# Kernel tuning notes

Measured on AMD Instinct MI355X. Metric: run time of the kernel, lower is better.

The kernel has to match this reference:

```python
import jax, jax.numpy as jnp
import numpy as np

N = 6144
M_VID = 1024
M_AUD = 128
APPERTURE = 20
EPS = 1e-6


def setup_inputs() -> dict:
    key = jax.random.key(0)
    ks = jax.random.split(key, 16)
    s = 0.02
    inp = {
        "x": jax.random.normal(ks[0], (1, N, M_VID), dtype=jnp.float32),
        "x_audio": jax.random.normal(ks[1], (1, N, M_AUD), dtype=jnp.float32),
        "seq_len": N,
        "audio_len": N,
        # video self-attention (torch Linear convention: W is [out, in])
        "Wk_v": jax.random.normal(ks[2], (M_VID, M_VID), dtype=jnp.float32) * s,
        "Wq_v": jax.random.normal(ks[3], (M_VID, M_VID), dtype=jnp.float32) * s,
        "Wv_v": jax.random.normal(ks[4], (M_VID, M_VID), dtype=jnp.float32) * s,
        "Wo_v": jax.random.normal(ks[5], (M_VID, M_VID), dtype=jnp.float32) * s,
        # audio self-attention
        "Wk_a": jax.random.normal(ks[6], (M_AUD, M_AUD), dtype=jnp.float32) * s,
        "Wq_a": jax.random.normal(ks[7], (M_AUD, M_AUD), dtype=jnp.float32) * s,
        "Wv_a": jax.random.normal(ks[8], (M_AUD, M_AUD), dtype=jnp.float32) * s,
        "Wo_a": jax.random.normal(ks[9], (M_AUD, M_AUD), dtype=jnp.float32) * s,
        # MLP head
        "ka_w": jax.random.normal(ks[10], (1024, M_VID + M_AUD), dtype=jnp.float32) * s,
        "ka_b": jnp.zeros((1024,), dtype=jnp.float32),
        "kd_w": jax.random.normal(ks[11], (1, 1024), dtype=jnp.float32) * s,
        "kd_b": jnp.zeros((1,), dtype=jnp.float32),
        # layer norms
        "ln_y_g": jnp.ones((M_VID,), dtype=jnp.float32),
        "ln_y_b": jnp.zeros((M_VID,), dtype=jnp.float32),
        "ln_ya_g": jnp.ones((M_AUD,), dtype=jnp.float32),
        "ln_ya_b": jnp.zeros((M_AUD,), dtype=jnp.float32),
        "ln_ka_g": jnp.ones((1024,), dtype=jnp.float32),
        "ln_ka_b": jnp.zeros((1024,), dtype=jnp.float32),
    }
    return inp


def _layer_norm(x, g, b):
    mu = jnp.mean(x, axis=-1, keepdims=True)
    var = jnp.mean((x - mu) ** 2, axis=-1, keepdims=True)
    return (x - mu) / jnp.sqrt(var + EPS) * g + b


def _self_attention(x, Wk, Wq, Wv, Wo):
    # x: [N, d]
    n = x.shape[0]
    K = x @ Wk.T
    Q = (x @ Wq.T) * 0.06
    V = x @ Wv.T
    logits = Q @ K.T  # [N, N]
    # keep only |i-j| < apperture (trimask masks |i-j| >= apperture)
    idx = jnp.arange(n)
    band = jnp.abs(idx[:, None] - idx[None, :]) < APPERTURE
    logits = jnp.where(band, logits, -jnp.inf)
    att = jax.nn.softmax(logits, axis=-1)  # [N, N]
    # torch: y = (V^T @ att)^T == att^T @ V  (note the transpose on att!)
    y = att.T @ V
    return y @ Wo.T, att


def reference(x, x_audio, seq_len, audio_len,
              Wk_v, Wq_v, Wv_v, Wo_v,
              Wk_a, Wq_a, Wv_a, Wo_a,
              ka_w, ka_b, kd_w, kd_b,
              ln_y_g, ln_y_b, ln_ya_g, ln_ya_b, ln_ka_g, ln_ka_b):
    m = x.shape[2]
    m_audio = x_audio.shape[2]
    xf = x.reshape(-1, m)            # [N, 1024]
    xa = x_audio.reshape(-1, m_audio)  # [N, 128]

    y, att_w = _self_attention(xf, Wk_v, Wq_v, Wv_v, Wo_v)
    y = _layer_norm(y + xf, ln_y_g, ln_y_b)

    ya, att_wa = _self_attention(xa, Wk_a, Wq_a, Wv_a, Wo_a)
    ya = _layer_norm(ya + xa, ln_ya_g, ln_ya_b)

    y_comb = jnp.concatenate((y, ya), axis=1)        # [N, 1152]
    att_comb = jnp.concatenate((att_w, att_wa), axis=1)  # [N, 2N]

    h = jax.nn.relu(y_comb @ ka_w.T + ka_b)
    h = _layer_norm(h, ln_ka_g, ln_ka_b)
    score = jax.nn.sigmoid(h @ kd_w.T + kd_b)  # [N, 1]
    score = score.reshape(1, -1)               # [1, N]
    return score, att_comb
```

## Files before the change

kernel.cpp:

```cpp
#include <hip/hip_runtime.h>
#include <stdint.h>

typedef unsigned short u16;
typedef unsigned int u32;
typedef __attribute__((ext_vector_type(8))) short bf16x8;
typedef __attribute__((ext_vector_type(4))) short s16x4;
typedef __attribute__((ext_vector_type(4))) float f32x4;
typedef __attribute__((ext_vector_type(2))) float f32x2;

#define DEV __device__ __forceinline__

DEV u16 f2bf(float f) {
  union { float f; unsigned u; } v; v.f = f;
  unsigned r = v.u + 0x7fffu + ((v.u >> 16) & 1u);
  return (u16)(r >> 16);
}
DEV float bf2f(u16 h) {
  union { u32 u; float f; } v; v.u = ((u32)h) << 16; return v.f;
}
DEV float lo16(u32 w) { union { u32 u; float f; } v; v.u = w << 16; return v.f; }
DEV float hi16(u32 w) { union { u32 u; float f; } v; v.u = w & 0xFFFF0000u; return v.f; }
DEV int imax(int a, int b) { return a > b ? a : b; }
DEV int imin(int a, int b) { return a < b ? a : b; }

DEV int xcd_swz(int b0, int nwg) {
  int q = nwg >> 3, r = nwg & 7, x = b0 & 7, l = b0 >> 3;
  return (x < r ? x * (q + 1) : r * (q + 1) + (x - r) * q) + l;
}

DEV void g2lds16(const u16* g, u16* l) {
  __builtin_amdgcn_global_load_lds(
      (const __attribute__((address_space(1))) void*)g,
      (__attribute__((address_space(3))) void*)l, 16, 0, 0);
}

DEV void write_att_row(int i, const float* __restrict__ bandV,
                       const float* __restrict__ bandA,
                       float* __restrict__ attBase, int N, int tid,
                       float* bw) {
  const int lo = imax(i - 19, 0);
  const int hi = imin(i + 19, N - 1);
  if (tid < 40) bw[tid] = bandV[i * 40 + tid];
  else if (tid < 80) bw[tid] = bandA[i * 40 + (tid - 40)];
  __syncthreads();
  const int nch = N / 4;
  const int cLo = lo >> 2, cHi = hi >> 2;
  f32x4* rowp = (f32x4*)(attBase + (size_t)i * 2 * N);
#pragma unroll 1
  for (int half = 0; half < 2; ++half) {
    const float* w = bw + half * 40;
    f32x4* rp = rowp + half * nch;
    for (int c = tid; c < nch; c += 256) {
      f32x4 o = {0.f, 0.f, 0.f, 0.f};
      if (c >= cLo && c <= cHi) {
        int col0 = c * 4;
#pragma unroll
        for (int e2 = 0; e2 < 4; ++e2) {
          int col = col0 + e2;
          if (col >= lo && col <= hi) o[e2] = w[col - lo];
        }
      }
      __builtin_nontemporal_store(o, &rp[c]);
    }
  }
}

#define NSEG 5
struct CastTab {
  const float* src[NSEG];
  u16* dst[NSEG];
  int start[NSEG + 1];
};

DEV void cast_block(const CastTab& t, int idx, int total4) {
  if (idx >= total4) return;
  int s = 0;
#pragma unroll
  for (int k = 1; k < NSEG; ++k)
    if (idx >= t.start[k]) s = k;
  int local = idx - t.start[s];
  f32x4 f = ((const f32x4*)t.src[s])[local];
  s16x4 o;
  o.x = (short)f2bf(f.x);
  o.y = (short)f2bf(f.y);
  o.z = (short)f2bf(f.z);
  o.w = (short)f2bf(f.w);
  ((s16x4*)t.dst[s])[local] = o;
}

struct TransTab {
  const float* src[6];
  u16* dst[6];
  int n[6];
  int start[7];
};

__global__ __launch_bounds__(256) void vas_prep(CastTab t, int total4,
                                                int castBlocks, TransTab tt) {
  if ((int)blockIdx.x < castBlocks) {
    cast_block(t, blockIdx.x * 256 + threadIdx.x, total4);
  } else {
    __shared__ float tl[32][33];
    int b = blockIdx.x - castBlocks;
    int s = 0;
#pragma unroll
    for (int k = 1; k < 6; ++k)
      if (b >= tt.start[k]) s = k;
    b -= tt.start[s];
    const float* src = tt.src[s];
    u16* dst = tt.dst[s];
    const int n = tt.n[s];
    const int tpr = n >> 5;
    const int tr = (b / tpr) * 32, tc = (b % tpr) * 32;
    const int lx = threadIdx.x & 31, ly = threadIdx.x >> 5;
#pragma unroll
    for (int r = 0; r < 4; ++r)
      tl[ly + r * 8][lx] = src[(size_t)(tr + ly + r * 8) * n + tc + lx];
    __syncthreads();
#pragma unroll
    for (int r = 0; r < 4; ++r)
      dst[(size_t)(tc + ly + r * 8) * n + tr + lx] = f2bf(tl[lx][ly + r * 8]);
  }
}

struct GemmP {
  const u16* A;
  const u16* W;
  void* C;
  const float* bias;
  int M, Nn, K, mode;
};

DEV void gemm_body(const GemmP& p, int bid, int tid,
                   u16 (*As)[128 * 32], u16 (*Ws)[128 * 32],
                   f32x4 (*acc)[4]) {
  const int lane = tid & 63;
  const int wave = tid >> 6;

  const int Mb = p.M >> 7, Nb = p.Nn >> 7;
  const int GM = 8;
  int per = GM * Nb;
  int g = bid / per;
  int rem = bid - g * per;
  int gm = imin(GM, Mb - g * GM);
  int mblk = g * GM + rem % gm;
  int nblk = rem / gm;
  const int m0 = mblk * 128;
  const int n0 = nblk * 128;
  const int wm = (wave >> 1) * 64;
  const int wn = (wave & 1) * 64;

  const int smat = wave >> 1;
  const int skh = wave & 1;
  const u16* ssrc = smat ? p.W : p.A;
  const int sbase = smat ? n0 : m0;
  u16* sdstBase = (smat ? &Ws[skh][0] : &As[skh][0]) + lane * 8;
  const int srow = lane >> 2;
  const int scol = (lane & 3) * 8;

  for (int k0 = 0; k0 < p.K; k0 += 64) {
#pragma unroll
    for (int u = 0; u < 8; ++u) {
      int r0 = u * 16;
      g2lds16(ssrc + (size_t)(sbase + r0 + srow) * p.K + (k0 + skh * 32 + scol),
              sdstBase + r0 * 32);
    }
    __syncthreads();
#pragma unroll
    for (int kk = 0; kk < 2; ++kk) {
      bf16x8 af[4], bfr[4];
#pragma unroll
      for (int t = 0; t < 4; ++t)
        af[t] = *(const bf16x8*)(&As[kk][0] + (wm + t * 16 + (lane & 15)) * 32 + (lane >> 4) * 8);
#pragma unroll
      for (int t = 0; t < 4; ++t)
        bfr[t] = *(const bf16x8*)(&Ws[kk][0] + (wn + t * 16 + (lane & 15)) * 32 + (lane >> 4) * 8);
#pragma unroll
      for (int mi = 0; mi < 4; ++mi)
#pragma unroll
        for (int ni = 0; ni < 4; ++ni)
          acc[mi][ni] = __builtin_amdgcn_mfma_f32_16x16x32_bf16(af[mi], bfr[ni], acc[mi][ni], 0, 0, 0);
    }
    __syncthreads();
  }
}

DEV void gemm_store(const GemmP& p, int bid, int tid, f32x4 (*acc)[4]) {
  const int lane = tid & 63;
  const int wave = tid >> 6;
  const int Mb = p.M >> 7, Nb = p.Nn >> 7;
  const int GM = 8;
  int per = GM * Nb;
  int g = bid / per;
  int rem = bid - g * per;
  int gm = imin(GM, Mb - g * GM);
  int mblk = g * GM + rem % gm;
  int nblk = rem / gm;
  const int m0 = mblk * 128;
  const int n0 = nblk * 128;
  const int wm = (wave >> 1) * 64;
  const int wn = (wave & 1) * 64;
#pragma unroll
  for (int mi = 0; mi < 4; ++mi) {
#pragma unroll
    for (int ni = 0; ni < 4; ++ni) {
      int col = n0 + wn + ni * 16 + (lane & 15);
      float bv = p.bias ? p.bias[col] : 0.f;
#pragma unroll
      for (int r = 0; r < 4; ++r) {
        int row = m0 + wm + mi * 16 + (lane >> 4) * 4 + r;
        float vv = acc[mi][ni][r] + bv;
        size_t idx = (size_t)row * p.Nn + col;
        if (p.mode == 0) ((float*)p.C)[idx] = vv;
        else if (p.mode == 1) ((u16*)p.C)[idx] = f2bf(fmaxf(vv, 0.f));
        else ((u16*)p.C)[idx] = f2bf(vv);
      }
    }
  }
}

__global__ __launch_bounds__(256) void vas_gemm4(
    GemmP p0, GemmP p1, GemmP p2, GemmP p3, int s1, int s2, int s3) {
  const int bs = xcd_swz(blockIdx.x, gridDim.x);
  GemmP p;
  int bid;
  if (bs < s1) { p = p0; bid = bs; }
  else if (bs < s2) { p = p1; bid = bs - s1; }
  else if (bs < s3) { p = p2; bid = bs - s2; }
  else { p = p3; bid = bs - s3; }

  __shared__ u16 As[2][128 * 32];
  __shared__ u16 Ws[2][128 * 32];
  f32x4 acc[4][4] = {};
  gemm_body(p, bid, threadIdx.x, As, Ws, acc);
  gemm_store(p, bid, threadIdx.x, acc);
}

__global__ __launch_bounds__(256) void vas_combine(
    GemmP p0, GemmP p1, GemmP p2, GemmP p3, int s1, int s2, int s3,
    int gb, CastTab ct, int total4) {
  if ((int)blockIdx.x >= gb) {
    cast_block(ct, (blockIdx.x - gb) * 256 + threadIdx.x, total4);
    return;
  }
  const int bs = xcd_swz(blockIdx.x, gb);
  GemmP p;
  int bid;
  if (bs < s1) { p = p0; bid = bs; }
  else if (bs < s2) { p = p1; bid = bs - s1; }
  else if (bs < s3) { p = p2; bid = bs - s2; }
  else { p = p3; bid = bs - s3; }

  __shared__ u16 As[2][128 * 32];
  __shared__ u16 Ws[2][128 * 32];
  f32x4 acc[4][4] = {};
  gemm_body(p, bid, threadIdx.x, As, Ws, acc);
  gemm_store(p, bid, threadIdx.x, acc);
}

__global__ __launch_bounds__(256) void vas_gemmh(
    GemmP p, const float* __restrict__ kw, const float* __restrict__ gw,
    float* __restrict__ part, int bh,
    const float* __restrict__ bandV, const float* __restrict__ bandA,
    float* __restrict__ attBase, int N) {
  const int tid = threadIdx.x;

  if ((int)blockIdx.x >= bh) {
    __shared__ float bw[80];
    write_att_row(blockIdx.x - bh, bandV, bandA, attBase, N, tid, bw);
    return;
  }

  const int bid = xcd_swz(blockIdx.x, bh);

  __shared__ u16 As[2][128 * 32];
  __shared__ u16 Ws[2][128 * 32];
  __shared__ float hp[2][128][3];
  const int lane = tid & 63;
  const int wave = tid >> 6;

  f32x4 acc[4][4] = {};
  gemm_body(p, bid, tid, As, Ws, acc);

  const int Mb = p.M >> 7, Nb = p.Nn >> 7;
  const int GM = 8;
  int per = GM * Nb;
  int g = bid / per;
  int rem = bid - g * per;
  int gm = imin(GM, Mb - g * GM);
  int mblk = g * GM + rem % gm;
  int nblk = rem / gm;
  const int m0 = mblk * 128;
  const int n0 = nblk * 128;
  const int wm = (wave >> 1) * 64;
  const int wn = (wave & 1) * 64;

  float kwg[4], bb[4];
#pragma unroll
  for (int ni = 0; ni < 4; ++ni) {
    int col = n0 + wn + ni * 16 + (lane & 15);
    kwg[ni] = kw[col] * gw[col];
    bb[ni] = p.bias ? p.bias[col] : 0.f;
  }
#pragma unroll
  for (int mi = 0; mi < 4; ++mi) {
#pragma unroll
    for (int r = 0; r < 4; ++r) {
      float s1 = 0.f, s2 = 0.f, dd = 0.f;
#pragma unroll
      for (int ni = 0; ni < 4; ++ni) {
        float vv = fmaxf(acc[mi][ni][r] + bb[ni], 0.f);
        s1 += vv;
        s2 += vv * vv;
        dd += vv * kwg[ni];
      }
#pragma unroll
      for (int off = 1; off < 16; off <<= 1) {
        s1 += __shfl_xor(s1, off);
        s2 += __shfl_xor(s2, off);
        dd += __shfl_xor(dd, off);
      }
      if ((lane & 15) == 0) {
        int row = wm + mi * 16 + (lane >> 4) * 4 + r;
        hp[wave & 1][row][0] = s1;
        hp[wave & 1][row][1] = s2;
        hp[wave & 1][row][2] = dd;
      }
    }
  }
  __syncthreads();
  if (tid < 128) {
    float* pp = part + ((size_t)(m0 + tid) * 8 + nblk) * 3;
    pp[0] = hp[0][tid][0] + hp[1][tid][0];
    pp[1] = hp[0][tid][1] + hp[1][tid][1];
    pp[2] = hp[0][tid][2] + hp[1][tid][2];
  }
}

__global__ __launch_bounds__(256) void vas_score(
    const float* __restrict__ part, const float* __restrict__ kw,
    const float* __restrict__ g, const float* __restrict__ b,
    const float* __restrict__ kb, float* __restrict__ score, int N) {
  const int tid = threadIdx.x, lane = tid & 63, wave = tid >> 6;
  __shared__ float shc[2][4];
  f32x4 kv = ((const f32x4*)kw)[tid];
  f32x4 gv = ((const f32x4*)g)[tid];
  f32x4 bv = ((const f32x4*)b)[tid];
  float c1 = kv.x * gv.x + kv.y * gv.y + kv.z * gv.z + kv.w * gv.w;
  float c2 = kv.x * bv.x + kv.y * bv.y + kv.z * bv.z + kv.w * bv.w;
#pragma unroll
  for (int off = 32; off; off >>= 1) {
    c1 += __shfl_xor(c1, off);
    c2 += __shfl_xor(c2, off);
  }
  if (lane == 0) { shc[0][wave] = c1; shc[1][wave] = c2; }
  __syncthreads();
  float C1 = shc[0][0] + shc[0][1] + shc[0][2] + shc[0][3];
  float C2 = shc[1][0] + shc[1][1] + shc[1][2] + shc[1][3];
  int row = blockIdx.x * 256 + tid;
  if (row < N) {
    const float* pp = part + (size_t)row * 24;
    float s1 = 0.f, s2 = 0.f, dd = 0.f;
#pragma unroll
    for (int k = 0; k < 8; ++k) {
      s1 += pp[k * 3];
      s2 += pp[k * 3 + 1];
      dd += pp[k * 3 + 2];
    }
    float mu = s1 / 1024.f;
    float var = s2 / 1024.f - mu * mu;
    float inv = rsqrtf(var + 1e-6f);
    float P = inv * dd - inv * mu * C1 + C2 + kb[0];
    score[row] = 1.f / (1.f + __expf(-P));
  }
}

__global__ __launch_bounds__(256) void vas_battn(
    const u16* __restrict__ Xv, const u16* __restrict__ Xa,
    const u16* __restrict__ KKVv, const u16* __restrict__ KKVa,
    float* __restrict__ bandV, float* __restrict__ bandA,
    int N, float scale, int vb) {
  const int lane = threadIdx.x & 63;
  const int wave = threadIdx.x >> 6;
  const bool video = blockIdx.x < (u32)vb;
  const int i = (video ? blockIdx.x : blockIdx.x - vb) * 4 + wave;
  const int lo = imax(i - 19, 0);
  const int hi = imin(i + 19, N - 1);
  const int nj = hi - lo + 1;
  float logit = 0.f;

  if (video) {
    float qf[16];
    const u16* qrow = Xv + (size_t)i * 1024;
#pragma unroll
    for (int c = 0; c < 2; ++c) {
      bf16x8 qv = *(const bf16x8*)(qrow + c * 512 + lane * 8);
      const u32* qw = (const u32*)&qv;
#pragma unroll
      for (int t = 0; t < 4; ++t) {
        qf[c * 8 + 2 * t] = lo16(qw[t]);
        qf[c * 8 + 2 * t + 1] = hi16(qw[t]);
      }
    }
#pragma unroll 2
    for (int s = 0; s < nj; ++s) {
      const u16* kr = KKVv + (size_t)(lo + s) * 2048;
      float p = 0.f;
#pragma unroll
      for (int c = 0; c < 2; ++c) {
        bf16x8 kv = *(const bf16x8*)(kr + c * 512 + lane * 8);
        const u32* kw = (const u32*)&kv;
#pragma unroll
        for (int t = 0; t < 4; ++t)
          p += lo16(kw[t]) * qf[c * 8 + 2 * t] + hi16(kw[t]) * qf[c * 8 + 2 * t + 1];
      }
#pragma unroll
      for (int off = 32; off; off >>= 1) p += __shfl_xor(p, off);
      if (lane == s) logit = p;
    }
  } else {
    u32 q = *(const u32*)(Xa + (size_t)i * 128 + lane * 2);
    float q0 = lo16(q), q1 = hi16(q);
#pragma unroll 2
    for (int s = 0; s < nj; ++s) {
      u32 k = *(const u32*)(KKVa + (size_t)(lo + s) * 256 + lane * 2);
      float p = lo16(k) * q0 + hi16(k) * q1;
#pragma unroll
      for (int off = 32; off; off >>= 1) p += __shfl_xor(p, off);
      if (lane == s) logit = p;
    }
  }

  logit *= scale;
  float v = (lane < nj) ? logit : -3.4e38f;
  float mx = v;
#pragma unroll
  for (int off = 32; off; off >>= 1) mx = fmaxf(mx, __shfl_xor(mx, off));
  float e = (lane < nj) ? __expf(v - mx) : 0.f;
  float den = e;
#pragma unroll
  for (int off = 32; off; off >>= 1) den += __shfl_xor(den, off);
  float att = (lane < nj) ? e / den : 0.f;
  float* band = video ? bandV : bandA;
  if (lane < 40) band[i * 40 + lane] = att;
}

#define JT 8
__global__ __launch_bounds__(256) void vas_apply_ln(
    const u16* __restrict__ KKVv, const u16* __restrict__ KKVa,
    const float* __restrict__ bandV, const float* __restrict__ bandA,
    const float* __restrict__ Xv, const float* __restrict__ Xa,
    const float* __restrict__ gv, const float* __restrict__ bv_,
    const float* __restrict__ ga, const float* __restrict__ ba,
    u16* __restrict__ out, int outStride, int N, int vb) {
  const int tid = threadIdx.x;
  __shared__ float a_sh[(JT + 38) * JT];
  __shared__ float red[2][JT][4];

  if (blockIdx.x < (u32)vb) {
    const int j0 = blockIdx.x * JT;
    const int base = j0 - 19;
    for (int idx = tid; idx < (JT + 38) * JT; idx += 256) {
      int s = idx / JT, jj = idx % JT;
      int i = base + s;
      int j = j0 + jj;
      float w = 0.f;
      if (i >= 0 && i < N) {
        int d = j - i;
        if (d > -20 && d < 20) w = bandV[i * 40 + (j - imax(i - 19, 0))];
      }
      a_sh[s * JT + jj] = w;
    }
    __syncthreads();

    f32x4 acc[JT] = {};
    const int sLo = imax(0, -base);
    const int sHi = imin(JT + 38, N - base);
    s16x4 nxt = *(const s16x4*)(KKVv + (size_t)(base + sLo) * 2048 + 1024 + tid * 4);
    for (int s = sLo; s < sHi; ++s) {
      s16x4 raw = nxt;
      if (s + 1 < sHi)
        nxt = *(const s16x4*)(KKVv + (size_t)(base + s + 1) * 2048 + 1024 + tid * 4);
      f32x4 vv;
      vv.x = bf2f((u16)raw.x);
      vv.y = bf2f((u16)raw.y);
      vv.z = bf2f((u16)raw.z);
      vv.w = bf2f((u16)raw.w);
#pragma unroll
      for (int jj = 0; jj < JT; ++jj) {
        float a = a_sh[s * JT + jj];
        acc[jj].x += a * vv.x;
        acc[jj].y += a * vv.y;
        acc[jj].z += a * vv.z;
        acc[jj].w += a * vv.w;
      }
    }

    const int lane = tid & 63, wave = tid >> 6;
#pragma unroll
    for (int jj = 0; jj < JT; ++jj) {
      f32x4 x4 = ((const f32x4*)(Xv + (size_t)(j0 + jj) * 1024))[tid];
      f32x4 v;
      v.x = acc[jj].x + x4.x;
      v.y = acc[jj].y + x4.y;
      v.z = acc[jj].z + x4.z;
      v.w = acc[jj].w + x4.w;
      acc[jj] = v;
      float s = v.x + v.y + v.z + v.w;
      float s2 = v.x * v.x + v.y * v.y + v.z * v.z + v.w * v.w;
#pragma unroll
      for (int off = 32; off; off >>= 1) {
        s += __shfl_xor(s, off);
        s2 += __shfl_xor(s2, off);
      }
      if (lane == 0) { red[0][jj][wave] = s; red[1][jj][wave] = s2; }
    }
    __syncthreads();
    f32x4 gg = ((const f32x4*)gv)[tid];
    f32x4 bb = ((const f32x4*)bv_)[tid];
#pragma unroll
    for (int jj = 0; jj < JT; ++jj) {
      float S = red[0][jj][0] + red[0][jj][1] + red[0][jj][2] + red[0][jj][3];
      float S2 = red[1][jj][0] + red[1][jj][1] + red[1][jj][2] + red[1][jj][3];
      float mu = S / 1024.f;
      float var = S2 / 1024.f - mu * mu;
      float inv = rsqrtf(var + 1e-6f);
      f32x4 v = acc[jj];
      s16x4 o;
      o.x = (short)f2bf((v.x - mu) * inv * gg.x + bb.x);
      o.y = (short)f2bf((v.y - mu) * inv * gg.y + bb.y);
      o.z = (short)f2bf((v.z - mu) * inv * gg.z + bb.z);
      o.w = (short)f2bf((v.w - mu) * inv * gg.w + bb.w);
      *(s16x4*)(out + (size_t)(j0 + jj) * outStride + tid * 4) = o;
    }
  } else {
    const int lane = tid & 63;
    const int wave = tid >> 6;
    const int j = (blockIdx.x - vb) * 4 + wave;
    const int lo = imax(j - 19, 0);
    const int hi = imin(j + 19, N - 1);
    const int ni = hi - lo + 1;
    float* aw = a_sh + wave * 40;
    if (lane < ni) {
      int i = lo + lane;
      aw[lane] = bandA[i * 40 + (j - imax(i - 19, 0))];
    }
    __syncthreads();
    f32x2 acc = {0.f, 0.f};
#pragma unroll 4
    for (int s = 0; s < ni; ++s) {
      float a = aw[s];
      u32 k = *(const u32*)(KKVa + (size_t)(lo + s) * 256 + 128 + lane * 2);
      acc.x += a * lo16(k);
      acc.y += a * hi16(k);
    }
    f32x2 x2 = *(const f32x2*)(Xa + (size_t)j * 128 + lane * 2);
    float vx = acc.x + x2.x;
    float vy = acc.y + x2.y;
    float s = vx + vy, s2 = vx * vx + vy * vy;
#pragma unroll
    for (int off = 32; off; off >>= 1) {
      s += __shfl_xor(s, off);
      s2 += __shfl_xor(s2, off);
    }
    float mu = s / 128.f;
    float var = s2 / 128.f - mu * mu;
    float inv = rsqrtf(var + 1e-6f);
    f32x2 g2 = *(const f32x2*)(ga + lane * 2);
    f32x2 b2 = *(const f32x2*)(ba + lane * 2);
    u32 o = (u32)f2bf((vx - mu) * inv * g2.x + b2.x) |
            ((u32)f2bf((vy - mu) * inv * g2.y + b2.y) << 16);
    *(u32*)(out + (size_t)j * outStride + 1024 + lane * 2) = o;
  }
}

extern "C" void kernel_launch(void* const* d_in, const int* in_sizes, int n_in,
                              void* d_out, int out_size, void* d_ws, size_t ws_size,
                              hipStream_t stream) {
  const float* x = (const float*)d_in[0];
  const float* xa = (const float*)d_in[1];
  const float* Wk_v = (const float*)d_in[4];
  const float* Wq_v = (const float*)d_in[5];
  const float* Wv_v = (const float*)d_in[6];
  const float* Wo_v = (const float*)d_in[7];
  const float* Wk_a = (const float*)d_in[8];
  const float* Wq_a = (const float*)d_in[9];
  const float* Wv_a = (const float*)d_in[10];
  const float* Wo_a = (const float*)d_in[11];
  const float* ka_w = (const float*)d_in[12];
  const float* ka_b = (const float*)d_in[13];
  const float* kd_w = (const float*)d_in[14];
  const float* kd_b = (const float*)d_in[15];
  const float* ln_y_g = (const float*)d_in[16];
  const float* ln_y_b = (const float*)d_in[17];
  const float* ln_ya_g = (const float*)d_in[18];
  const float* ln_ya_b = (const float*)d_in[19];
  const float* ln_ka_g = (const float*)d_in[20];
  const float* ln_ka_b = (const float*)d_in[21];

  const int N = in_sizes[0] / 1024;
  const int MV = 1024, MA = 128, MH = 1152;

  char* wsb = (char*)d_ws;
  size_t off = 0;
  auto alloc = [&](size_t bytes) -> void* {
    void* p = wsb + off;
    off += (bytes + 255) & ~(size_t)255;
    return p;
  };
  u16* xf_b   = (u16*)alloc((size_t)N * MV * 2);
  u16* xa_b   = (u16*)alloc((size_t)N * MA * 2);
  u16* wov_b  = (u16*)alloc((size_t)MV * MV * 2);
  u16* woa_b  = (u16*)alloc((size_t)MA * MA * 2);
  u16* wqTv   = (u16*)alloc((size_t)MV * MV * 2);
  u16* wkTv   = (u16*)alloc((size_t)MV * MV * 2);
  u16* wvTv   = (u16*)alloc((size_t)MV * MV * 2);
  u16* wqTa   = (u16*)alloc((size_t)MA * MA * 2);
  u16* wkTa   = (u16*)alloc((size_t)MA * MA * 2);
  u16* wvTa   = (u16*)alloc((size_t)MA * MA * 2);
  u16* wWv    = (u16*)alloc((size_t)2 * MV * MV * 2);
  u16* wWa    = (u16*)alloc((size_t)2 * MA * MA * 2);
  u16* kaw_b  = (u16*)alloc((size_t)1024 * MH * 2);
  u16* KKVv   = (u16*)alloc((size_t)N * 2 * MV * 2);
  u16* KKVa   = (u16*)alloc((size_t)N * 2 * MA * 2);
  float* bandV = (float*)alloc((size_t)N * 40 * 4);
  float* bandA = (float*)alloc((size_t)N * 40 * 4);
  u16* ycomb_b = (u16*)alloc((size_t)N * MH * 2);
  float* part_b = (float*)alloc((size_t)N * 8 * 3 * 4);

  float* dout = (float*)d_out;
  float* attBase = dout + N;

  {
    CastTab t;
    for (int k = 0; k < NSEG; ++k) { t.src[k] = nullptr; t.dst[k] = nullptr; }
    int c = 0, cum = 0;
    auto seg = [&](const float* s, u16* d, size_t n) {
      t.src[c] = s; t.dst[c] = d; t.start[c] = cum; cum += (int)(n / 4); ++c;
    };
    seg(Wo_v, wov_b, (size_t)MV * MV);
    seg(Wo_a, woa_b, (size_t)MA * MA);
    for (int k = c; k <= NSEG; ++k) t.start[k] = cum;
    int castBlocks = (cum + 255) / 256;

    TransTab tt;
    int c2 = 0, cum2 = 0;
    auto seg2 = [&](const float* s, u16* d, int n) {
      tt.src[c2] = s; tt.dst[c2] = d; tt.n[c2] = n; tt.start[c2] = cum2;
      cum2 += (n / 32) * (n / 32); ++c2;
    };
    seg2(Wq_v, wqTv, MV);
    seg2(Wk_v, wkTv, MV);
    seg2(Wv_v, wvTv, MV);
    seg2(Wq_a, wqTa, MA);
    seg2(Wk_a, wkTa, MA);
    seg2(Wv_a, wvTa, MA);
    tt.start[c2] = cum2;

    vas_prep<<<castBlocks + cum2, 256, 0, stream>>>(t, cum, castBlocks, tt);
  }

  {
    GemmP gv = {wqTv, wkTv, wWv, nullptr, MV, MV, MV, 2};
    GemmP uv = {wov_b, wvTv, wWv + (size_t)MV * MV, nullptr, MV, MV, MV, 2};
    GemmP ga = {wqTa, wkTa, wWa, nullptr, MA, MA, MA, 2};
    GemmP ua = {woa_b, wvTa, wWa + (size_t)MA * MA, nullptr, MA, MA, MA, 2};
    int bg = (MV / 128) * (MV / 128);
    int gb = 2 * bg + 2;

    CastTab ct;
    for (int k = 0; k < NSEG; ++k) { ct.src[k] = nullptr; ct.dst[k] = nullptr; }
    int c = 0, cum = 0;
    auto seg = [&](const float* s, u16* d, size_t n) {
      ct.src[c] = s; ct.dst[c] = d; ct.start[c] = cum; cum += (int)(n / 4); ++c;
    };
    seg(x, xf_b, (size_t)N * MV);
    seg(xa, xa_b, (size_t)N * MA);
    seg(ka_w, kaw_b, (size_t)1024 * MH);
    for (int k = c; k <= NSEG; ++k) ct.start[k] = cum;
    int castBlocks = (cum + 255) / 256;

    vas_combine<<<gb + castBlocks, 256, 0, stream>>>(
        gv, uv, ga, ua, bg, 2 * bg, 2 * bg + 1, gb, ct, cum);
  }

  {
    GemmP pv = {xf_b, wWv, KKVv, nullptr, N, 2 * MV, MV, 2};
    GemmP pa = {xa_b, wWa, KKVa, nullptr, N, 2 * MA, MA, 2};
    int bv = (N / 128) * (2 * MV / 128);
    int ba = (N / 128) * (2 * MA / 128);
    vas_gemm4<<<bv + ba, 256, 0, stream>>>(pv, pa, pa, pa, bv, bv + ba, bv + ba);
  }

  vas_battn<<<N / 2, 256, 0, stream>>>(xf_b, xa_b, KKVv, KKVa, bandV, bandA,
                                       N, 0.06f, N / 4);

  vas_apply_ln<<<N / JT + N / 4, 256, 0, stream>>>(
      KKVv, KKVa, bandV, bandA, x, xa,
      ln_y_g, ln_y_b, ln_ya_g, ln_ya_b, ycomb_b, MH, N, N / JT);

  {
    GemmP ph = {ycomb_b, kaw_b, nullptr, ka_b, N, 1024, MH, 1};
    int bh = (N / 128) * (1024 / 128);
    vas_gemmh<<<bh + N, 256, 0, stream>>>(ph, kd_w, ln_ka_g, part_b, bh,
                                          bandV, bandA, attBase, N);
  }

  vas_score<<<(N + 255) / 256, 256, 0, stream>>>(
      part_b, kd_w, ln_ka_g, ln_ka_b, kd_b, dout, N);
}
```

Before: 526.8 us.

## Spread zero-fill of attention output across earlier kernels, write band separately

Splits the large attention-matrix output write into zero-filling off-band regions and writing only the narrow band values. Zero fills, which do not depend on attention results, are distributed as extra blocks in the combine, projection GEMM and head GEMM launches (rows split at fixed offsets) so they can overlap compute. The band itself is written at the end by a compact per-row kernel using one wave per row. This risks contending for memory bandwidth with the GEMMs, and the fixed split points are tuned for the given sequence length.

```diff
diff --git a/kernel.cpp b/kernel.cpp
--- a/kernel.cpp
+++ b/kernel.cpp
@@ -34,35 +34,44 @@
       (__attribute__((address_space(3))) void*)l, 16, 0, 0);
 }
 
-DEV void write_att_row(int i, const float* __restrict__ bandV,
-                       const float* __restrict__ bandA,
-                       float* __restrict__ attBase, int N, int tid,
-                       float* bw) {
+
+DEV void fill_att_row_zeros(int i, float* __restrict__ attBase, int N,
+                            int tid) {
   const int lo = imax(i - 19, 0);
   const int hi = imin(i + 19, N - 1);
-  if (tid < 40) bw[tid] = bandV[i * 40 + tid];
-  else if (tid < 80) bw[tid] = bandA[i * 40 + (tid - 40)];
-  __syncthreads();
+  const int cLo = lo >> 2, cHi = hi >> 2;
   const int nch = N / 4;
-  const int cLo = lo >> 2, cHi = hi >> 2;
+  f32x4 z = {0.f, 0.f, 0.f, 0.f};
   f32x4* rowp = (f32x4*)(attBase + (size_t)i * 2 * N);
-#pragma unroll 1
-  for (int half = 0; half < 2; ++half) {
-    const float* w = bw + half * 40;
-    f32x4* rp = rowp + half * nch;
-    for (int c = tid; c < nch; c += 256) {
-      f32x4 o = {0.f, 0.f, 0.f, 0.f};
-      if (c >= cLo && c <= cHi) {
-        int col0 = c * 4;
-#pragma unroll
-        for (int e2 = 0; e2 < 4; ++e2) {
-          int col = col0 + e2;
-          if (col >= lo && col <= hi) o[e2] = w[col - lo];
-        }
-      }
-      __builtin_nontemporal_store(o, &rp[c]);
-    }
-  }
+  for (int c = tid; c < 2 * nch; c += 256) {
+    int cc = c >= nch ? c - nch : c;
+    if (cc >= cLo && cc <= cHi) continue;
+    __builtin_nontemporal_store(z, &rowp[c]);
+  }
+}
+
+DEV void write_att_band4(int i0, const float* __restrict__ bandV,
+                         const float* __restrict__ bandA,
+                         float* __restrict__ attBase, int N, int tid) {
+  const int lane = tid & 63, wave = tid >> 6;
+  const int i = i0 + wave;
+  const int lo = imax(i - 19, 0);
+  const int hi = imin(i + 19, N - 1);
+  const int cLo = lo >> 2, cHi = hi >> 2, ncb = cHi - cLo + 1;
+  const int nch = N / 4;
+  const bool aud = lane >= 32;
+  const int l = aud ? lane - 32 : lane;
+  if (l >= ncb || (!aud && lane >= 16)) return;
+  const float* band = aud ? bandA : bandV;
+  f32x4* rowp = (f32x4*)(attBase + (size_t)i * 2 * N) + (aud ? nch : 0);
+  int c = cLo + l;
+  f32x4 o;
+#pragma unroll
+  for (int e = 0; e < 4; ++e) {
+    int col = c * 4 + e;
+    o[e] = (col >= lo && col <= hi) ? band[i * 40 + (col - lo)] : 0.f;
+  }
+  __builtin_nontemporal_store(o, &rowp[c]);
 }
 
 #define NSEG 5
@@ -220,8 +229,14 @@
 }
 
 __global__ __launch_bounds__(256) void vas_gemm4(
-    GemmP p0, GemmP p1, GemmP p2, GemmP p3, int s1, int s2, int s3) {
-  const int bs = xcd_swz(blockIdx.x, gridDim.x);
+    GemmP p0, GemmP p1, GemmP p2, GemmP p3, int s1, int s2, int s3,
+    int gemmBlocks, float* attBase, int N, int fillRow0) {
+  if ((int)blockIdx.x >= gemmBlocks) {
+    fill_att_row_zeros(fillRow0 + (blockIdx.x - gemmBlocks), attBase, N,
+                       threadIdx.x);
+    return;
+  }
+  const int bs = xcd_swz(blockIdx.x, gemmBlocks);
   GemmP p;
   int bid;
   if (bs < s1) { p = p0; bid = bs; }
@@ -238,7 +253,12 @@
 
 __global__ __launch_bounds__(256) void vas_combine(
     GemmP p0, GemmP p1, GemmP p2, GemmP p3, int s1, int s2, int s3,
-    int gb, CastTab ct, int total4) {
+    int gb, CastTab ct, int total4, int castBlocks,
+    float* attBase, int N) {
+  if ((int)blockIdx.x >= gb + castBlocks) {
+    fill_att_row_zeros(blockIdx.x - gb - castBlocks, attBase, N, threadIdx.x);
+    return;
+  }
   if ((int)blockIdx.x >= gb) {
     cast_block(ct, (blockIdx.x - gb) * 256 + threadIdx.x, total4);
     return;
@@ -260,14 +280,18 @@
 
 __global__ __launch_bounds__(256) void vas_gemmh(
     GemmP p, const float* __restrict__ kw, const float* __restrict__ gw,
-    float* __restrict__ part, int bh,
+    float* __restrict__ part, int bh, int nfill, int fillRow0,
     const float* __restrict__ bandV, const float* __restrict__ bandA,
     float* __restrict__ attBase, int N) {
   const int tid = threadIdx.x;
 
+  if ((int)blockIdx.x >= bh + nfill) {
+    write_att_band4((blockIdx.x - bh - nfill) * 4, bandV, bandA, attBase, N,
+                    tid);
+    return;
+  }
   if ((int)blockIdx.x >= bh) {
-    __shared__ float bw[80];
-    write_att_row(blockIdx.x - bh, bandV, bandA, attBase, N, tid, bw);
+    fill_att_row_zeros(fillRow0 + (blockIdx.x - bh), attBase, N, tid);
     return;
   }
 
@@ -600,6 +624,8 @@
 
   const int N = in_sizes[0] / 1024;
   const int MV = 1024, MA = 128, MH = 1152;
+  const int F1 = 768;
+  const int F2 = 3584;
 
   char* wsb = (char*)d_ws;
   size_t off = 0;
@@ -680,8 +706,9 @@
     for (int k = c; k <= NSEG; ++k) ct.start[k] = cum;
     int castBlocks = (cum + 255) / 256;
 
-    vas_combine<<<gb + castBlocks, 256, 0, stream>>>(
-        gv, uv, ga, ua, bg, 2 * bg, 2 * bg + 1, gb, ct, cum);
+    vas_combine<<<gb + castBlocks + F1, 256, 0, stream>>>(
+        gv, uv, ga, ua, bg, 2 * bg, 2 * bg + 1, gb, ct, cum, castBlocks,
+        attBase, N);
   }
 
   {
@@ -689,7 +716,9 @@
     GemmP pa = {xa_b, wWa, KKVa, nullptr, N, 2 * MA, MA, 2};
     int bv = (N / 128) * (2 * MV / 128);
     int ba = (N / 128) * (2 * MA / 128);
-    vas_gemm4<<<bv + ba, 256, 0, stream>>>(pv, pa, pa, pa, bv, bv + ba, bv + ba);
+    int gb = bv + ba;
+    vas_gemm4<<<gb + (F2 - F1), 256, 0, stream>>>(
+        pv, pa, pa, pa, bv, gb, gb, gb, attBase, N, F1);
   }
 
   vas_battn<<<N / 2, 256, 0, stream>>>(xf_b, xa_b, KKVv, KKVa, bandV, bandA,
@@ -702,8 +731,9 @@
   {
     GemmP ph = {ycomb_b, kaw_b, nullptr, ka_b, N, 1024, MH, 1};
     int bh = (N / 128) * (1024 / 128);
-    vas_gemmh<<<bh + N, 256, 0, stream>>>(ph, kd_w, ln_ka_g, part_b, bh,
-                                          bandV, bandA, attBase, N);
+    int nfill = N - F2;
+    vas_gemmh<<<bh + nfill + N / 4, 256, 0, stream>>>(
+        ph, kd_w, ln_ka_g, part_b, bh, nfill, F2, bandV, bandA, attBase, N);
   }
 
   vas_score<<<(N + 255) / 256, 256, 0, stream>>>(
```

Measured after the change: 531.5 us. About the same (+0.9%).
